# Kernel tuning notes

Hardware: AMD Instinct MI355X
Metric: run time of the kernel (lower is better)

The kernel has to match this reference:

```python
import jax, jax.numpy as jnp
import numpy as np

B, T, D, NH, DK = 2, 2048, 1024, 16, 64
EPS = 1e-6

def proj_H(z):
    return z - z.mean(axis=-1, keepdims=True)

def to_clr(p):
    return proj_H(jnp.log(p + EPS))

def setup_inputs() -> dict:
    key = jax.random.key(0)
    ks = jax.random.split(key, 9)
    p = jax.random.uniform(ks[0], (B, T, D), dtype=jnp.float32)
    # xavier_uniform with gain=0.8 for square-ish [in,out] matrices
    def xavier(k, fan_in, fan_out):
        bound = 0.8 * np.sqrt(6.0 / (fan_in + fan_out))
        return jax.random.uniform(k, (fan_in, fan_out), minval=-bound, maxval=bound, dtype=jnp.float32)
    H = NH * DK
    Wq = xavier(ks[1], D, H); bq = jnp.zeros((H,), jnp.float32)
    Wk = xavier(ks[2], D, H); bk = jnp.zeros((H,), jnp.float32)
    Wv = xavier(ks[3], D, H); bv = jnp.zeros((H,), jnp.float32)
    Wo = xavier(ks[4], H, D); bo = jnp.zeros((D,), jnp.float32)
    return {"p": p, "Wq": Wq, "bq": bq, "Wk": Wk, "bk": bk,
            "Wv": Wv, "bv": bv, "Wo": Wo, "bo": bo}

def reference(p, Wq, bq, Wk, bk, Wv, bv, Wo, bo):
    z = to_clr(p)                                   # [B,T,D]
    # projections with H-projection epilogue, reshaped to [B,T,NH,DK]
    q = proj_H(z @ Wq + bq).reshape(B, T, NH, DK)
    k = proj_H(z @ Wk + bk).reshape(B, T, NH, DK)
    v = proj_H(z @ Wv + bv).reshape(B, T, NH, DK)
    att = jnp.einsum('bihd,bjhd->bhij', q, k) / jnp.sqrt(jnp.float32(DK))
    w = jax.nn.softmax(att, axis=-1)                # dropout is identity in eval
    z_out = jnp.einsum('bhij,bjhd->bihd', w, v).reshape(B, T, NH * DK)
    z_out = proj_H(z_out @ Wo + bo)
    return jax.nn.softmax(z_out, axis=-1)           # from_clr
```

## Files before the change

### kernel.cpp

```cpp
#include <hip/hip_runtime.h>

typedef unsigned short u16;
typedef __attribute__((ext_vector_type(8))) short short8_t;
typedef __attribute__((ext_vector_type(8))) _Float16 half8_t;
typedef __attribute__((ext_vector_type(4))) float f32x4;
typedef __attribute__((ext_vector_type(16))) float f32x16;
typedef __attribute__((ext_vector_type(4))) int int4v;

#define BB    2
#define TT    2048
#define DD    1024
#define NHEAD 16
#define DKH   64
#define HH    1024
#define MR    4096
#define CLR_EPS 1e-6f
#define QSCALE_CONST 0.18033688011112042f

#define O_WQKVT  0ull
#define O_WOT    6291456ull
#define O_WMEAN  8388608ull
#define O_BQKV   8404992ull
#define O_BO     8417280ull
#define O_Z      8421376ull
#define O_QKV    16809984ull
#define O_VT     41975808ull
#define O_ZOUT   50364416ull
#define O_LOGITS O_QKV

__device__ __forceinline__ u16 f2h(float f) {
  _Float16 h = (_Float16)f;
  return __builtin_bit_cast(u16, h);
}
__device__ __forceinline__ float h2f(u16 x) {
  return (float)__builtin_bit_cast(_Float16, x);
}

__device__ __forceinline__ f32x4 mfma16(short8_t a, short8_t b, f32x4 c) {
  return __builtin_amdgcn_mfma_f32_16x16x32_f16(
      __builtin_bit_cast(half8_t, a), __builtin_bit_cast(half8_t, b), c, 0, 0, 0);
}
__device__ __forceinline__ f32x16 mfma32(short8_t a, short8_t b, f32x16 c) {
  return __builtin_amdgcn_mfma_f32_32x32x16_f16(
      __builtin_bit_cast(half8_t, a), __builtin_bit_cast(half8_t, b), c, 0, 0, 0);
}

typedef const __attribute__((address_space(1))) unsigned int as1_u32_t;
typedef __attribute__((address_space(3))) unsigned int as3_u32_t;

__device__ __forceinline__ void async16(const void* g, void* l) {
  __builtin_amdgcn_global_load_lds((as1_u32_t*)g, (as3_u32_t*)l, 16, 0, 0);
}

__device__ __forceinline__ short8_t ldfrag(const u16* buf, int row, int kh, int lane) {
  const int byte = (row * 128 + ((kh * 32 + ((lane >> 4) << 3)) << 1)) ^ ((row & 7) << 4);
  return *(const short8_t*)((const char*)buf + byte);
}

__global__ __launch_bounds__(256) void wprep_mean(
    const float* __restrict__ Wq, const float* __restrict__ Wk,
    const float* __restrict__ Wv, const float* __restrict__ Wo,
    const float* __restrict__ bq, const float* __restrict__ bk,
    const float* __restrict__ bv, const float* __restrict__ bo,
    float* __restrict__ wmean, float* __restrict__ bqkv_p, float* __restrict__ bo_p) {
  __shared__ float sb[4];
  const int bid = blockIdx.x, tid = threadIdx.x;
  if (bid < 4096) {
    const int m = bid >> 10, d = bid & 1023;
    const float* Wm = (m == 0) ? Wq : (m == 1) ? Wk : (m == 2) ? Wv : Wo;
    float4 x = ((const float4*)(Wm + (size_t)d * 1024))[tid];
    float s = x.x + x.y + x.z + x.w;
    #pragma unroll
    for (int dd = 32; dd; dd >>= 1) s += __shfl_xor(s, dd);
    if ((tid & 63) == 0) sb[tid >> 6] = s;
    __syncthreads();
    if (tid == 0) wmean[bid] = (sb[0] + sb[1] + sb[2] + sb[3]) * (1.f / 1024.f);
  } else {
    const int j = bid - 4096;
    const float* bb = (j == 0) ? bq : (j == 1) ? bk : (j == 2) ? bv : bo;
    float4 x = ((const float4*)bb)[tid];
    float s = x.x + x.y + x.z + x.w;
    #pragma unroll
    for (int dd = 32; dd; dd >>= 1) s += __shfl_xor(s, dd);
    if ((tid & 63) == 0) sb[tid >> 6] = s;
    __syncthreads();
    const float mean = (sb[0] + sb[1] + sb[2] + sb[3]) * (1.f / 1024.f);
    float* dst = (j < 3) ? (bqkv_p + j * 1024) : bo_p;
    float4 o = {x.x - mean, x.y - mean, x.z - mean, x.w - mean};
    ((float4*)dst)[tid] = o;
  }
}

__global__ __launch_bounds__(256) void wprep_trans(
    const float* __restrict__ Wq, const float* __restrict__ Wk,
    const float* __restrict__ Wv, const float* __restrict__ Wo,
    const float* __restrict__ wmean, u16* __restrict__ wqkvt, u16* __restrict__ wot) {
  __shared__ float tl[64][65];
  const int tj = blockIdx.x, ti = blockIdx.y, m = blockIdx.z;
  const int tid = threadIdx.x;
  const float* Wm = (m == 0) ? Wq : (m == 1) ? Wk : (m == 2) ? Wv : Wo;
  const int d0 = ti * 64, h0 = tj * 64;
  #pragma unroll
  for (int rr = 0; rr < 4; ++rr) {
    const int r = (tid >> 4) + rr * 16;
    float4 x = *(const float4*)(Wm + (size_t)(d0 + r) * 1024 + h0 + ((tid & 15) << 2));
    const float mu = wmean[m * 1024 + d0 + r];
    tl[r][(tid & 15) * 4 + 0] = x.x - mu;
    tl[r][(tid & 15) * 4 + 1] = x.y - mu;
    tl[r][(tid & 15) * 4 + 2] = x.z - mu;
    tl[r][(tid & 15) * 4 + 3] = x.w - mu;
  }
  __syncthreads();
  #pragma unroll
  for (int rr = 0; rr < 2; ++rr) {
    const int hh = (tid >> 3) + rr * 32;
    const int cd = (tid & 7) << 3;
    short8_t v;
    #pragma unroll
    for (int i = 0; i < 8; ++i) v[i] = (short)f2h(tl[cd + i][hh]);
    u16* dst = (m < 3) ? (wqkvt + ((size_t)(m * 1024 + h0 + hh)) * 1024 + d0 + cd)
                       : (wot + ((size_t)(h0 + hh)) * 1024 + d0 + cd);
    *(short8_t*)dst = v;
  }
}

__global__ __launch_bounds__(256) void clr_kernel(const float* __restrict__ p, u16* __restrict__ z) {
  __shared__ float sb[4];
  const int r = blockIdx.x, tid = threadIdx.x;
  float4 x = ((const float4*)(p + (size_t)r * 1024))[tid];
  float l0 = __logf(x.x + CLR_EPS), l1 = __logf(x.y + CLR_EPS);
  float l2 = __logf(x.z + CLR_EPS), l3 = __logf(x.w + CLR_EPS);
  float s = l0 + l1 + l2 + l3;
  #pragma unroll
  for (int dd = 32; dd; dd >>= 1) s += __shfl_xor(s, dd);
  if ((tid & 63) == 0) sb[tid >> 6] = s;
  __syncthreads();
  const float mu = (sb[0] + sb[1] + sb[2] + sb[3]) * (1.f / 1024.f);
  ushort4 o;
  o.x = f2h(l0 - mu); o.y = f2h(l1 - mu); o.z = f2h(l2 - mu); o.w = f2h(l3 - mu);
  ((ushort4*)(z + (size_t)r * 1024))[tid] = o;
}

__global__ __launch_bounds__(256, 2) void gemm_qkv_8ph(
    const u16* __restrict__ A, const u16* __restrict__ Bt, const float* __restrict__ bias,
    u16* __restrict__ qkv, u16* __restrict__ vt) {
  __shared__ u16 As[2][128 * 64];
  __shared__ u16 Bs[2][192 * 64];
  const int tid = threadIdx.x, lane = tid & 63, w = tid >> 6;
  const int wm = w >> 1, wn = w & 1;
  const int id = blockIdx.x;
  const int x = id & 7, idx = id >> 3;
  const int mt = (x & 3) * 8 + (idx & 7);
  const int nt = (x >> 2) * 8 + (idx >> 3);
  const int m0 = mt * 128, n0 = nt * 192;
  const int srow = tid >> 3, schk = tid & 7;
  const int l15 = lane & 15, lg4 = (lane >> 4) << 2;

  f32x4 acc[4][6] = {};

  auto stA = [&](int k0, int buf) {
    #pragma unroll
    for (int u = 0; u < 4; ++u) {
      const int r = srow + u * 32;
      const int c = k0 + ((schk ^ (r & 7)) << 3);
      async16(A + (size_t)(m0 + r) * 1024 + c, &As[buf][r * 64 + schk * 8]);
    }
  };
  auto stB = [&](int k0, int buf) {
    #pragma unroll
    for (int u = 0; u < 6; ++u) {
      const int r = srow + u * 32;
      const int c = k0 + ((schk ^ (r & 7)) << 3);
      async16(Bt + (size_t)(n0 + r) * 1024 + c, &Bs[buf][r * 64 + schk * 8]);
    }
  };

  stA(0, 0); stB(0, 0);
  asm volatile("s_waitcnt vmcnt(0)" ::: "memory");
  __builtin_amdgcn_s_barrier();

  short8_t afr[4], bfr[6];
  for (int t = 0; t < 16; ++t) {
    const int cur = t & 1;
    const int k0n = ((t + 1) & 15) * 64;
    const u16* Ab = &As[cur][0];
    const u16* Bb_ = &Bs[cur][0];

    #pragma unroll
    for (int j = 0; j < 6; ++j) bfr[j] = ldfrag(Bb_, wn * 96 + j * 16 + l15, 0, lane);
    #pragma unroll
    for (int i = 0; i < 4; ++i) afr[i] = ldfrag(Ab, wm * 64 + i * 16 + l15, 0, lane);
    stA(k0n, cur ^ 1); stB(k0n, cur ^ 1);
    __builtin_amdgcn_s_barrier();
    asm volatile("s_waitcnt lgkmcnt(0)" ::: "memory");
    __builtin_amdgcn_sched_barrier(0);
    __builtin_amdgcn_s_setprio(1);
    #pragma unroll
    for (int i = 0; i < 4; ++i)
      #pragma unroll
      for (int j = 0; j < 6; ++j)
        acc[i][j] = mfma16(afr[i], bfr[j], acc[i][j]);
    __builtin_amdgcn_s_setprio(0);
    __builtin_amdgcn_s_barrier();

    #pragma unroll
    for (int j = 0; j < 6; ++j) bfr[j] = ldfrag(Bb_, wn * 96 + j * 16 + l15, 1, lane);
    #pragma unroll
    for (int i = 0; i < 4; ++i) afr[i] = ldfrag(Ab, wm * 64 + i * 16 + l15, 1, lane);
    __builtin_amdgcn_s_barrier();
    asm volatile("s_waitcnt lgkmcnt(0)" ::: "memory");
    __builtin_amdgcn_sched_barrier(0);
    __builtin_amdgcn_s_setprio(1);
    #pragma unroll
    for (int i = 0; i < 4; ++i)
      #pragma unroll
      for (int j = 0; j < 6; ++j)
        acc[i][j] = mfma16(afr[i], bfr[j], acc[i][j]);
    __builtin_amdgcn_s_setprio(0);
    asm volatile("s_waitcnt vmcnt(0)" ::: "memory");
    __builtin_amdgcn_s_barrier();
  }

  #pragma unroll
  for (int j = 0; j < 6; ++j) {
    const int col = n0 + wn * 96 + j * 16 + l15;
    const float bb = bias[col];
    if (col < 2048) {
      const float sc = (col < 1024) ? QSCALE_CONST : 1.0f;
      #pragma unroll
      for (int i = 0; i < 4; ++i) {
        const int rowb = m0 + wm * 64 + i * 16 + lg4;
        #pragma unroll
        for (int r = 0; r < 4; ++r)
          qkv[(size_t)(rowb + r) * 3072 + col] = f2h((acc[i][j][r] + bb) * sc);
      }
    } else {
      const int h = (col - 2048) >> 6, dk = col & 63;
      #pragma unroll
      for (int i = 0; i < 4; ++i) {
        const int rowb = m0 + wm * 64 + i * 16 + lg4;
        const int b = rowb >> 11, tq = rowb & 2047;
        const int k5 = tq & 31;
        const int pos = (tq & ~31) + (k5 & 16) + ((k5 & 4) << 1) + ((k5 & 8) >> 1);
        ushort4 pk;
        pk.x = f2h(acc[i][j][0] + bb);
        pk.y = f2h(acc[i][j][1] + bb);
        pk.z = f2h(acc[i][j][2] + bb);
        pk.w = f2h(acc[i][j][3] + bb);
        *(ushort4*)(vt + ((size_t)((b * NHEAD + h) * 64 + dk)) * TT + pos) = pk;
      }
    }
  }
}

__global__ __launch_bounds__(256, 3) void gemm_bt(
    const u16* __restrict__ A, const u16* __restrict__ Bt, const float* __restrict__ bias,
    float* __restrict__ Cout, int Ndim, int Kdim) {
  __shared__ u16 As[2][128 * 64];
  __shared__ u16 Bs[2][64 * 64];
  const int tid = threadIdx.x;
  const int lane = tid & 63, wid = tid >> 6;
  const int m0 = blockIdx.y * 128, n0 = blockIdx.x * 64;
  const int wm = wid >> 1, wn = wid & 1;
  const int srow = tid >> 3, schk = tid & 7;
  f32x4 acc[4][2] = {};

  auto STG = [&](int k0, int buf) {
    #pragma unroll
    for (int rr = 0; rr < 4; ++rr) {
      const int row = srow + rr * 32;
      const int gcol = k0 + ((schk ^ (row & 7)) << 3);
      async16(A + (size_t)(m0 + row) * Kdim + gcol, &As[buf][row * 64 + schk * 8]);
      if (rr < 2)
        async16(Bt + (size_t)(n0 + row) * Kdim + gcol, &Bs[buf][row * 64 + schk * 8]);
    }
  };

  STG(0, 0);
  asm volatile("s_waitcnt vmcnt(0)" ::: "memory");
  __builtin_amdgcn_s_barrier();

  const int ntk = Kdim >> 6;
  for (int t = 0; t < ntk; ++t) {
    const int cur = t & 1;
    STG((((t + 1) & (ntk - 1))) << 6, cur ^ 1);
    #pragma unroll
    for (int kk = 0; kk < 2; ++kk) {
      short8_t af[4], bf[2];
      #pragma unroll
      for (int i = 0; i < 4; ++i)
        af[i] = ldfrag(&As[cur][0], wm * 64 + i * 16 + (lane & 15), kk, lane);
      #pragma unroll
      for (int j = 0; j < 2; ++j)
        bf[j] = ldfrag(&Bs[cur][0], wn * 32 + j * 16 + (lane & 15), kk, lane);
      __builtin_amdgcn_s_setprio(1);
      #pragma unroll
      for (int i = 0; i < 4; ++i)
        #pragma unroll
        for (int j = 0; j < 2; ++j)
          acc[i][j] = mfma16(af[i], bf[j], acc[i][j]);
      __builtin_amdgcn_s_setprio(0);
    }
    asm volatile("s_waitcnt vmcnt(0)" ::: "memory");
    __builtin_amdgcn_s_barrier();
  }

  #pragma unroll
  for (int j = 0; j < 2; ++j) {
    const int col = n0 + wn * 32 + j * 16 + (lane & 15);
    const float bb = bias[col];
    #pragma unroll
    for (int i = 0; i < 4; ++i) {
      const int rowb = m0 + wm * 64 + i * 16 + ((lane >> 4) << 2);
      #pragma unroll
      for (int r = 0; r < 4; ++r)
        Cout[(size_t)(rowb + r) * Ndim + col] = acc[i][j][r] + bb;
    }
  }
}

__global__ __launch_bounds__(512, 2) void attn_kernel(
    const u16* __restrict__ qkv, const u16* __restrict__ vt, u16* __restrict__ zout) {
  __shared__ char smem[65536];
  const int id = blockIdx.x;
  const int qb = (id >> 3) & 7;
  const int bh = (id & 7) * 4 + (id >> 6);
  const int b = bh >> 4, h = bh & 15;
  const int tid = threadIdx.x, lane = tid & 63, w = tid >> 6;
  const int qw = w & 3, ks = w >> 2;
  const int hl = lane >> 5, l31 = lane & 31;
  const int swz = (l31 & 7) << 4;
  const int q0 = qb * 256 + qw * 64;

  short8_t qf[2][4];
  #pragma unroll
  for (int qt = 0; qt < 2; ++qt)
    #pragma unroll
    for (int c = 0; c < 4; ++c)
      qf[qt][c] = *(const short8_t*)(qkv + (size_t)(b * TT + q0 + qt * 32 + l31) * 3072
                                     + h * 64 + c * 16 + hl * 8);

  const int sr0 = qw * 16 + (lane >> 3);
  const int schk = lane & 7;
  const int scol = (schk ^ (sr0 & 7)) << 3;
  const int dof = sr0 * 128 + schk * 16;
  char* kls = smem + ks * 16384;
  char* vls = smem + 32768 + ks * 16384;
  const u16* kg = qkv + 1024 + (size_t)h * 64;
  const u16* vg = vt + ((size_t)(b * NHEAD + h) * 64 + sr0) * (size_t)TT;

  {
    const int kbase = ks * 1024;
    async16(kg + (size_t)(b * TT + kbase + sr0) * 3072 + scol, kls + dof);
    async16(kg + (size_t)(b * TT + kbase + sr0 + 8) * 3072 + scol, kls + dof + 1024);
    async16(vg + kbase + scol, vls + dof);
    async16(vg + (size_t)8 * TT + kbase + scol, vls + dof + 1024);
  }

  f32x16 o[2][2] = {};
  f32x16 lb[2] = {};
  short8_t ones;
  #pragma unroll
  for (int i = 0; i < 8; ++i) ones[i] = (short)0x3C00;

  for (int it = 0; it < 16; ++it) {
    __syncthreads();
    if (it < 15) {
      const int kbase = ks * 1024 + (it + 1) * 64;
      const int bo = ((it + 1) & 1) * 8192;
      async16(kg + (size_t)(b * TT + kbase + sr0) * 3072 + scol, kls + bo + dof);
      async16(kg + (size_t)(b * TT + kbase + sr0 + 8) * 3072 + scol, kls + bo + dof + 1024);
      async16(vg + kbase + scol, vls + bo + dof);
      async16(vg + (size_t)8 * TT + kbase + scol, vls + bo + dof + 1024);
    }
    const char* Kb = kls + (it & 1) * 8192;
    const char* Vb = vls + (it & 1) * 8192;

    f32x16 s[2][2] = {};
    __builtin_amdgcn_s_setprio(1);
    #pragma unroll
    for (int kt = 0; kt < 2; ++kt) {
      #pragma unroll
      for (int c = 0; c < 4; ++c) {
        const int krow = kt * 32 + l31;
        const short8_t kfr = *(const short8_t*)(Kb + krow * 128 + ((c * 32 + hl * 16) ^ swz));
        s[kt][0] = mfma32(kfr, qf[0][c], s[kt][0]);
        s[kt][1] = mfma32(kfr, qf[1][c], s[kt][1]);
      }
    }
    __builtin_amdgcn_s_setprio(0);

    #pragma unroll
    for (int kt = 0; kt < 2; ++kt)
      #pragma unroll
      for (int qt = 0; qt < 2; ++qt)
        #pragma unroll
        for (int r = 0; r < 16; ++r) {
          float pv;
          asm("v_exp_f32 %0, %1" : "=v"(pv) : "v"(s[kt][qt][r]));
          s[kt][qt][r] = pv;
        }

    #pragma unroll
    for (int kt = 0; kt < 2; ++kt) {
      #pragma unroll
      for (int cc = 0; cc < 2; ++cc) {
        short8_t pa[2];
        #pragma unroll
        for (int qt = 0; qt < 2; ++qt) {
          int w0 = __builtin_bit_cast(int, __builtin_amdgcn_cvt_pkrtz(s[kt][qt][8 * cc + 0], s[kt][qt][8 * cc + 1]));
          int w1 = __builtin_bit_cast(int, __builtin_amdgcn_cvt_pkrtz(s[kt][qt][8 * cc + 2], s[kt][qt][8 * cc + 3]));
          int w2 = __builtin_bit_cast(int, __builtin_amdgcn_cvt_pkrtz(s[kt][qt][8 * cc + 4], s[kt][qt][8 * cc + 5]));
          int w3 = __builtin_bit_cast(int, __builtin_amdgcn_cvt_pkrtz(s[kt][qt][8 * cc + 6], s[kt][qt][8 * cc + 7]));
          int4v fw = {w0, w1, w2, w3};
          pa[qt] = __builtin_bit_cast(short8_t, fw);
          lb[qt] = mfma32(pa[qt], ones, lb[qt]);
        }
        const int cb = kt * 64 + cc * 32 + hl * 16;
        __builtin_amdgcn_s_setprio(1);
        #pragma unroll
        for (int dkt = 0; dkt < 2; ++dkt) {
          const int vrow = dkt * 32 + l31;
          const short8_t vfr = *(const short8_t*)(Vb + vrow * 128 + (cb ^ swz));
          o[0][dkt] = mfma32(pa[0], vfr, o[0][dkt]);
          o[1][dkt] = mfma32(pa[1], vfr, o[1][dkt]);
        }
        __builtin_amdgcn_s_setprio(0);
      }
    }
  }

  __syncthreads();
  const int slot = qw * 64 + lane;
  if (ks == 1) {
    u16* ro = (u16*)(smem + slot * 136);
    #pragma unroll
    for (int qt = 0; qt < 2; ++qt)
      #pragma unroll
      for (int dkt = 0; dkt < 2; ++dkt)
        #pragma unroll
        for (int r = 0; r < 16; ++r)
          ro[(qt * 2 + dkt) * 16 + r] = f2h(o[qt][dkt][r]);
    u16* rl = (u16*)(smem + 36864 + slot * 72);
    #pragma unroll
    for (int qt = 0; qt < 2; ++qt)
      #pragma unroll
      for (int r = 0; r < 16; ++r)
        rl[qt * 16 + r] = f2h(lb[qt][r]);
  }
  __syncthreads();
  if (ks == 0) {
    const u16* ro = (const u16*)(smem + slot * 136);
    const u16* rl = (const u16*)(smem + 36864 + slot * 72);
    #pragma unroll
    for (int qt = 0; qt < 2; ++qt) {
      #pragma unroll
      for (int r = 0; r < 16; ++r) lb[qt][r] += h2f(rl[qt * 16 + r]);
      #pragma unroll
      for (int dkt = 0; dkt < 2; ++dkt)
        #pragma unroll
        for (int r = 0; r < 16; ++r) o[qt][dkt][r] += h2f(ro[(qt * 2 + dkt) * 16 + r]);
    }
    #pragma unroll
    for (int qt = 0; qt < 2; ++qt) {
      float rlv[16];
      #pragma unroll
      for (int r = 0; r < 16; ++r) rlv[r] = 1.f / lb[qt][r];
      #pragma unroll
      for (int dkt = 0; dkt < 2; ++dkt) {
        const int col = h * 64 + dkt * 32 + l31;
        #pragma unroll
        for (int r = 0; r < 16; ++r) {
          const int rowg = b * TT + q0 + qt * 32 + (r & 3) + 8 * (r >> 2) + 4 * hl;
          zout[(size_t)rowg * 1024 + col] = f2h(o[qt][dkt][r] * rlv[r]);
        }
      }
    }
  }
}

__global__ __launch_bounds__(256) void softmax_rows(const float* __restrict__ logits,
                                                    float* __restrict__ out) {
  __shared__ float sb[8];
  const int r = blockIdx.x, tid = threadIdx.x;
  float4 x = ((const float4*)(logits + (size_t)r * 1024))[tid];
  float mx = fmaxf(fmaxf(x.x, x.y), fmaxf(x.z, x.w));
  #pragma unroll
  for (int dd = 32; dd; dd >>= 1) mx = fmaxf(mx, __shfl_xor(mx, dd));
  if ((tid & 63) == 0) sb[tid >> 6] = mx;
  __syncthreads();
  mx = fmaxf(fmaxf(sb[0], sb[1]), fmaxf(sb[2], sb[3]));
  const float e0 = __expf(x.x - mx), e1 = __expf(x.y - mx);
  const float e2 = __expf(x.z - mx), e3 = __expf(x.w - mx);
  float s = e0 + e1 + e2 + e3;
  #pragma unroll
  for (int dd = 32; dd; dd >>= 1) s += __shfl_xor(s, dd);
  __syncthreads();
  if ((tid & 63) == 0) sb[4 + (tid >> 6)] = s;
  __syncthreads();
  s = sb[4] + sb[5] + sb[6] + sb[7];
  const float inv = 1.f / s;
  float4 o = {e0 * inv, e1 * inv, e2 * inv, e3 * inv};
  ((float4*)(out + (size_t)r * 1024))[tid] = o;
}

extern "C" void kernel_launch(void* const* d_in, const int* in_sizes, int n_in,
                              void* d_out, int out_size, void* d_ws, size_t ws_size,
                              hipStream_t stream) {
  (void)in_sizes; (void)n_in; (void)out_size; (void)ws_size;
  const float* p  = (const float*)d_in[0];
  const float* Wq = (const float*)d_in[1];
  const float* bq = (const float*)d_in[2];
  const float* Wk = (const float*)d_in[3];
  const float* bk = (const float*)d_in[4];
  const float* Wv = (const float*)d_in[5];
  const float* bv = (const float*)d_in[6];
  const float* Wo = (const float*)d_in[7];
  const float* bo = (const float*)d_in[8];
  float* out = (float*)d_out;

  char* ws = (char*)d_ws;
  u16*   wqkvt  = (u16*)(ws + O_WQKVT);
  u16*   wot    = (u16*)(ws + O_WOT);
  float* wmean  = (float*)(ws + O_WMEAN);
  float* bqkv_p = (float*)(ws + O_BQKV);
  float* bo_p   = (float*)(ws + O_BO);
  u16*   z      = (u16*)(ws + O_Z);
  u16*   qkv    = (u16*)(ws + O_QKV);
  u16*   vt     = (u16*)(ws + O_VT);
  u16*   zoutb  = (u16*)(ws + O_ZOUT);
  float* logits = (float*)(ws + O_LOGITS);

  wprep_mean<<<4100, 256, 0, stream>>>(Wq, Wk, Wv, Wo, bq, bk, bv, bo, wmean, bqkv_p, bo_p);
  wprep_trans<<<dim3(16, 16, 4), 256, 0, stream>>>(Wq, Wk, Wv, Wo, wmean, wqkvt, wot);
  clr_kernel<<<MR, 256, 0, stream>>>(p, z);
  gemm_qkv_8ph<<<512, 256, 0, stream>>>(z, wqkvt, bqkv_p, qkv, vt);
  attn_kernel<<<256, 512, 0, stream>>>(qkv, vt, zoutb);
  gemm_bt<<<dim3(1024 / 64, MR / 128), 256, 0, stream>>>(zoutb, wot, bo_p, logits, 1024, 1024);
  softmax_rows<<<MR, 256, 0, stream>>>(logits, out);
}
```

Measured before the change: 119.3 us.

## Retile QKV GEMM to 128x128x32 tiles with simpler single-phase pipeline

Measured after the change: 122.0 us. 1.02x slower.

```diff
diff --git a/kernel.cpp b/kernel.cpp
--- a/kernel.cpp
+++ b/kernel.cpp
@@ -54,6 +54,11 @@
 
 __device__ __forceinline__ short8_t ldfrag(const u16* buf, int row, int kh, int lane) {
   const int byte = (row * 128 + ((kh * 32 + ((lane >> 4) << 3)) << 1)) ^ ((row & 7) << 4);
+  return *(const short8_t*)((const char*)buf + byte);
+}
+
+__device__ __forceinline__ short8_t ldfrag32(const u16* buf, int row, int lane) {
+  const int byte = row * 64 + ((((lane >> 4) << 4)) ^ ((row & 3) << 4));
   return *(const short8_t*)((const char*)buf + byte);
 }
 
@@ -141,89 +146,61 @@
   ((ushort4*)(z + (size_t)r * 1024))[tid] = o;
 }
 
-__global__ __launch_bounds__(256, 2) void gemm_qkv_8ph(
+__global__ __launch_bounds__(256, 3) void gemm_qkv_8ph(
     const u16* __restrict__ A, const u16* __restrict__ Bt, const float* __restrict__ bias,
     u16* __restrict__ qkv, u16* __restrict__ vt) {
-  __shared__ u16 As[2][128 * 64];
-  __shared__ u16 Bs[2][192 * 64];
+  __shared__ u16 As[2][128 * 32];
+  __shared__ u16 Bs[2][128 * 32];
   const int tid = threadIdx.x, lane = tid & 63, w = tid >> 6;
   const int wm = w >> 1, wn = w & 1;
   const int id = blockIdx.x;
-  const int x = id & 7, idx = id >> 3;
-  const int mt = (x & 3) * 8 + (idx & 7);
-  const int nt = (x >> 2) * 8 + (idx >> 3);
-  const int m0 = mt * 128, n0 = nt * 192;
-  const int srow = tid >> 3, schk = tid & 7;
+  const int x = id & 7, j0 = id >> 3;
+  const int mt = (x & 3) * 8 + (j0 & 7);
+  const int nt = (x >> 2) * 12 + (j0 >> 3);
+  const int m0 = mt * 128, n0 = nt * 128;
+  const int srow = tid >> 2, schk = tid & 3;
   const int l15 = lane & 15, lg4 = (lane >> 4) << 2;
 
-  f32x4 acc[4][6] = {};
-
-  auto stA = [&](int k0, int buf) {
-    #pragma unroll
-    for (int u = 0; u < 4; ++u) {
-      const int r = srow + u * 32;
-      const int c = k0 + ((schk ^ (r & 7)) << 3);
-      async16(A + (size_t)(m0 + r) * 1024 + c, &As[buf][r * 64 + schk * 8]);
+  f32x4 acc[4][4] = {};
+
+  auto STG = [&](int k0, int buf) {
+    #pragma unroll
+    for (int u = 0; u < 2; ++u) {
+      const int r = srow + u * 64;
+      const int c = k0 + ((schk ^ (r & 3)) << 3);
+      async16(A + (size_t)(m0 + r) * 1024 + c, &As[buf][r * 32 + schk * 8]);
+      async16(Bt + (size_t)(n0 + r) * 1024 + c, &Bs[buf][r * 32 + schk * 8]);
     }
   };
-  auto stB = [&](int k0, int buf) {
-    #pragma unroll
-    for (int u = 0; u < 6; ++u) {
-      const int r = srow + u * 32;
-      const int c = k0 + ((schk ^ (r & 7)) << 3);
-      async16(Bt + (size_t)(n0 + r) * 1024 + c, &Bs[buf][r * 64 + schk * 8]);
-    }
-  };
-
-  stA(0, 0); stB(0, 0);
+
+  STG(0, 0);
   asm volatile("s_waitcnt vmcnt(0)" ::: "memory");
   __builtin_amdgcn_s_barrier();
 
-  short8_t afr[4], bfr[6];
-  for (int t = 0; t < 16; ++t) {
+  for (int t = 0; t < 32; ++t) {
     const int cur = t & 1;
-    const int k0n = ((t + 1) & 15) * 64;
-    const u16* Ab = &As[cur][0];
-    const u16* Bb_ = &Bs[cur][0];
-
-    #pragma unroll
-    for (int j = 0; j < 6; ++j) bfr[j] = ldfrag(Bb_, wn * 96 + j * 16 + l15, 0, lane);
-    #pragma unroll
-    for (int i = 0; i < 4; ++i) afr[i] = ldfrag(Ab, wm * 64 + i * 16 + l15, 0, lane);
-    stA(k0n, cur ^ 1); stB(k0n, cur ^ 1);
-    __builtin_amdgcn_s_barrier();
-    asm volatile("s_waitcnt lgkmcnt(0)" ::: "memory");
-    __builtin_amdgcn_sched_barrier(0);
+    STG(((t + 1) & 31) * 32, cur ^ 1);
+    short8_t af[4], bf[4];
+    #pragma unroll
+    for (int i = 0; i < 4; ++i)
+      af[i] = ldfrag32(&As[cur][0], wm * 64 + i * 16 + l15, lane);
+    #pragma unroll
+    for (int j = 0; j < 4; ++j)
+      bf[j] = ldfrag32(&Bs[cur][0], wn * 64 + j * 16 + l15, lane);
     __builtin_amdgcn_s_setprio(1);
     #pragma unroll
     for (int i = 0; i < 4; ++i)
       #pragma unroll
-      for (int j = 0; j < 6; ++j)
-        acc[i][j] = mfma16(afr[i], bfr[j], acc[i][j]);
-    __builtin_amdgcn_s_setprio(0);
-    __builtin_amdgcn_s_barrier();
-
-    #pragma unroll
-    for (int j = 0; j < 6; ++j) bfr[j] = ldfrag(Bb_, wn * 96 + j * 16 + l15, 1, lane);
-    #pragma unroll
-    for (int i = 0; i < 4; ++i) afr[i] = ldfrag(Ab, wm * 64 + i * 16 + l15, 1, lane);
-    __builtin_amdgcn_s_barrier();
-    asm volatile("s_waitcnt lgkmcnt(0)" ::: "memory");
-    __builtin_amdgcn_sched_barrier(0);
-    __builtin_amdgcn_s_setprio(1);
-    #pragma unroll
-    for (int i = 0; i < 4; ++i)
-      #pragma unroll
-      for (int j = 0; j < 6; ++j)
-        acc[i][j] = mfma16(afr[i], bfr[j], acc[i][j]);
+      for (int j = 0; j < 4; ++j)
+        acc[i][j] = mfma16(af[i], bf[j], acc[i][j]);
     __builtin_amdgcn_s_setprio(0);
     asm volatile("s_waitcnt vmcnt(0)" ::: "memory");
     __builtin_amdgcn_s_barrier();
   }
 
   #pragma unroll
-  for (int j = 0; j < 6; ++j) {
-    const int col = n0 + wn * 96 + j * 16 + l15;
+  for (int j = 0; j < 4; ++j) {
+    const int col = n0 + wn * 64 + j * 16 + l15;
     const float bb = bias[col];
     if (col < 2048) {
       const float sc = (col < 1024) ? QSCALE_CONST : 1.0f;
@@ -534,7 +511,7 @@
   wprep_mean<<<4100, 256, 0, stream>>>(Wq, Wk, Wv, Wo, bq, bk, bv, bo, wmean, bqkv_p, bo_p);
   wprep_trans<<<dim3(16, 16, 4), 256, 0, stream>>>(Wq, Wk, Wv, Wo, wmean, wqkvt, wot);
   clr_kernel<<<MR, 256, 0, stream>>>(p, z);
-  gemm_qkv_8ph<<<512, 256, 0, stream>>>(z, wqkvt, bqkv_p, qkv, vt);
+  gemm_qkv_8ph<<<768, 256, 0, stream>>>(z, wqkvt, bqkv_p, qkv, vt);
   attn_kernel<<<256, 512, 0, stream>>>(qkv, vt, zoutb);
   gemm_bt<<<dim3(1024 / 64, MR / 128), 256, 0, stream>>>(zoutb, wot, bo_p, logits, 1024, 1024);
   softmax_rows<<<MR, 256, 0, stream>>>(logits, out);
```
